# Performance work log

Measured on AMD Instinct MI355X. Metric: run time of the kernel, lower is better.

Reference implementation:

```python
import jax, jax.numpy as jnp
import numpy as np

N = 50000   # nodes
E = 800000  # edges
D = 128     # node_channels


def setup_inputs() -> dict:
    key = jax.random.key(0)
    ks = jax.random.split(key, 16)
    s = 1.0 / np.sqrt(D)
    inp = {
        "x": jax.random.normal(ks[0], (N, D), dtype=jnp.float32),
        "edge_index": jax.random.randint(ks[1], (2, E), 0, N, dtype=jnp.int64),
        "eps": jax.random.normal(ks[2], (N, D), dtype=jnp.float32),
    }
    names = ["1", "2", "mu", "logstd", "5", "6"]
    for i, nm in enumerate(names):
        inp[f"W{nm}"] = jax.random.normal(ks[3 + 2 * i], (D, D), dtype=jnp.float32) * s
        inp[f"b{nm}"] = jnp.zeros((D,), dtype=jnp.float32)
    return inp


def _gcn_norm(edge_index, num_nodes):
    # add self-loops, then symmetric normalization deg^{-1/2} (A+I) deg^{-1/2}
    loop = jnp.arange(num_nodes, dtype=edge_index.dtype)
    src = jnp.concatenate([edge_index[0], loop])
    dst = jnp.concatenate([edge_index[1], loop])
    deg = jax.ops.segment_sum(jnp.ones_like(src, dtype=jnp.float32), dst,
                              num_segments=num_nodes)
    dis = jnp.where(deg > 0, jax.lax.rsqrt(deg), 0.0)
    norm = dis[src] * dis[dst]  # [E + N]
    return src, dst, norm


def _gcn(x, W, b, src, dst, norm, num_nodes):
    h = x @ W                              # [N, D] small GEMM
    msg = h[src] * norm[:, None]           # gather + scale, [E+N, D]
    out = jax.ops.segment_sum(msg, dst, num_segments=num_nodes)  # scatter-add
    return out + b


def reference(x, edge_index, eps, W1, b1, W2, b2, Wmu, bmu, Wlogstd, blogstd,
              W5, b5, W6, b6):
    num_nodes = x.shape[0]
    src, dst, norm = _gcn_norm(edge_index, num_nodes)
    g = lambda h, W, b: _gcn(h, W, b, src, dst, norm, num_nodes)

    nodes = jax.nn.relu(g(x, W1, b1))
    nodes = jax.nn.relu(g(nodes, W2, b2))
    mu = g(nodes, Wmu, bmu)
    logstd = g(nodes, Wlogstd, blogstd)
    # reparametrize (training mode), divider = 10
    nodes = mu + eps * jnp.exp(logstd) / 10.0
    nodes = jax.nn.relu(g(nodes, W5, b5))
    nodes = jax.nn.relu(g(nodes, W6, b6))
    return nodes
```

## Files before the change

### kernel.cpp

```cpp
#include <hip/hip_runtime.h>
#include <hip/hip_bf16.h>
#include <cstdint>
#include <cstddef>

#define D 128
#define NWG 200

typedef _Float16 f16;
typedef f16 f16x2 __attribute__((ext_vector_type(2)));
typedef f16 f16x4 __attribute__((ext_vector_type(4)));
typedef f16 f16x8 __attribute__((ext_vector_type(8)));
typedef float f32x4 __attribute__((ext_vector_type(4)));
typedef unsigned short u16;

static inline size_t align256(size_t x){ return (x + 255) & ~(size_t)255; }

__device__ __forceinline__ int detect_is64(const void* ei){
  const int* e32 = (const int*)ei;
  int probe = e32[2 * (threadIdx.x & 31) + 1];
  return (__ballot(probe != 0) == 0ULL) ? 1 : 0;
}

__device__ __forceinline__ void load_edge(const void* ei, int E, int is64, int e, int& s, int& d){
  if (is64) {
    const long long* p = (const long long*)ei;
    s = (int)p[e]; d = (int)p[(size_t)E + e];
  } else {
    const int* p = (const int*)ei;
    s = p[e]; d = p[(size_t)E + e];
  }
}

__global__ __launch_bounds__(256) void passA_hist(
    const void* __restrict__ ei, int E,
    int* __restrict__ glob_hist, int NB){
  __shared__ int cnt[256];
  int t = threadIdx.x, wg = blockIdx.x;
  int is64 = detect_is64(ei);
  cnt[t] = 0;
  __syncthreads();
  int chunk = (E + NWG - 1) / NWG;
  int lo = wg * chunk, hi = min(lo + chunk, E);
  for (int e = lo + t; e < hi; e += 256){
    int s, d;
    load_edge(ei, E, is64, e, s, d);
    atomicAdd(&cnt[d >> 8], 1);
  }
  __syncthreads();
  for (int b = t; b < NB; b += 256)
    glob_hist[b * NWG + wg] = cnt[b];
}

__global__ void scan_partial(const int* __restrict__ src, int* __restrict__ dst,
                             int* __restrict__ blockSums, int L){
  __shared__ int sd[256];
  int t = threadIdx.x;
  int base = blockIdx.x * 1024 + t * 4;
  int v[4]; int s = 0;
  #pragma unroll
  for (int j = 0; j < 4; ++j){ v[j] = (base + j < L) ? src[base + j] : 0; s += v[j]; }
  sd[t] = s; __syncthreads();
  for (int off = 1; off < 256; off <<= 1){
    int x = (t >= off) ? sd[t - off] : 0;
    __syncthreads();
    sd[t] += x;
    __syncthreads();
  }
  int run = sd[t] - s;
  #pragma unroll
  for (int j = 0; j < 4; ++j){
    if (base + j < L) dst[base + j] = run;
    run += v[j];
  }
  if (t == 255) blockSums[blockIdx.x] = sd[255];
}

__global__ void scan_blocksums(int* __restrict__ blockSums, int nblk){
  __shared__ int sd[256];
  int t = threadIdx.x;
  int v = (t < nblk) ? blockSums[t] : 0;
  sd[t] = v; __syncthreads();
  for (int off = 1; off < 256; off <<= 1){
    int x = (t >= off) ? sd[t - off] : 0;
    __syncthreads();
    sd[t] += x;
    __syncthreads();
  }
  if (t < nblk) blockSums[t] = sd[t] - v;
}

__global__ __launch_bounds__(256) void passB_scatter(
    const void* __restrict__ ei, int E,
    const int* __restrict__ bucketOff, const int* __restrict__ blockSums,
    int NB, unsigned* __restrict__ packed){
  __shared__ int cur[256];
  int t = threadIdx.x, wg = blockIdx.x;
  int is64 = detect_is64(ei);
  for (int b = t; b < NB; b += 256){
    int i = b * NWG + wg;
    cur[b] = bucketOff[i] + blockSums[i >> 10];
  }
  __syncthreads();
  int chunk = (E + NWG - 1) / NWG;
  int lo = wg * chunk, hi = min(lo + chunk, E);
  for (int e = lo + t; e < hi; e += 256){
    int s, d;
    load_edge(ei, E, is64, e, s, d);
    int pos = atomicAdd(&cur[d >> 8], 1);
    packed[pos] = (unsigned)s | ((unsigned)(d & 255) << 16);
  }
}

__global__ __launch_bounds__(256) void passC_csr(
    const unsigned* __restrict__ packed, const int* __restrict__ bucketOff,
    const int* __restrict__ blockSums, int NB, int N, int E,
    int* __restrict__ rowptr, float* __restrict__ dis, u16* __restrict__ csr_src){
  __shared__ int degl[256];
  __shared__ int sd[256];
  __shared__ int cur[256];
  int t = threadIdx.x, b = blockIdx.x;
  int i0 = b * NWG, i1 = (b + 1) * NWG;
  int begin = bucketOff[i0] + blockSums[i0 >> 10];
  int endb  = (b == NB - 1) ? E : (bucketOff[i1] + blockSums[i1 >> 10]);
  degl[t] = 0;
  __syncthreads();
  for (int i = begin + t; i < endb; i += 256)
    atomicAdd(&degl[(packed[i] >> 16) & 255], 1);
  __syncthreads();
  int dv = degl[t];
  sd[t] = dv; __syncthreads();
  for (int off = 1; off < 256; off <<= 1){
    int x = (t >= off) ? sd[t - off] : 0;
    __syncthreads();
    sd[t] += x;
    __syncthreads();
  }
  int localOff = sd[t] - dv;
  int v = b * 256 + t;
  if (v < N){
    rowptr[v] = begin + localOff;
    dis[v] = rsqrtf((float)(dv + 1));
  }
  if (b == NB - 1 && t == 0) rowptr[N] = E;
  cur[t] = begin + localOff;
  __syncthreads();
  for (int i = begin + t; i < endb; i += 256){
    unsigned p = packed[i];
    int pos = atomicAdd(&cur[(p >> 16) & 255], 1);
    csr_src[pos] = (u16)(p & 0xFFFFu);
  }
}

__global__ void cast_scale(const float* __restrict__ in, const float* __restrict__ dis,
                           f16* __restrict__ out, int n4){
  int i = blockIdx.x * blockDim.x + threadIdx.x;
  if (i >= n4) return;
  float dv = dis[i >> 5];
  float4 v = ((const float4*)in)[i];
  f16x4 o; o[0]=(f16)(v.x*dv); o[1]=(f16)(v.y*dv); o[2]=(f16)(v.z*dv); o[3]=(f16)(v.w*dv);
  ((f16x4*)out)[i] = o;
}

__global__ void prep_w(const float* __restrict__ Wa, const float* __restrict__ Wb,
                       const float* __restrict__ Wc, const float* __restrict__ Wd,
                       const float* __restrict__ We, const float* __restrict__ Wf,
                       f16* __restrict__ Wt){
  int i = blockIdx.x * 256 + threadIdx.x;
  int w = i >> 14, rem = i & 16383;
  int n = rem >> 7, k = rem & 127;
  const float* Wp = (w==0)?Wa:(w==1)?Wb:(w==2)?Wc:(w==3)?Wd:(w==4)?We:Wf;
  Wt[i] = (f16)Wp[k*128 + n];
}

__global__ __launch_bounds__(256) void agg16(
    const f16* __restrict__ in, f16* __restrict__ out,
    const int* __restrict__ rowptr, const u16* __restrict__ csr_src,
    const float* __restrict__ dis, int N){
  int v = blockIdx.x * 4 + (threadIdx.x >> 6);
  if (v >= N) return;
  int c2 = (threadIdx.x & 63) * 2;
  float dv = dis[v];
  int beg = rowptr[v], end = rowptr[v + 1];
  f16x2 sv = *(const f16x2*)&in[(size_t)v * D + c2];
  float acc0 = (float)sv[0], acc1 = (float)sv[1];
  int e = beg;
  for (; e + 15 < end; e += 16){
    f16x2 h[16];
    #pragma unroll
    for (int j = 0; j < 16; ++j){
      unsigned u = __builtin_nontemporal_load(&csr_src[e + j]);
      h[j] = *(const f16x2*)&in[(size_t)u * D + c2];
    }
    #pragma unroll
    for (int j = 0; j < 16; ++j){ acc0 += (float)h[j][0]; acc1 += (float)h[j][1]; }
  }
  int rem = end - e;
  if (rem > 0){
    int last = end - 1;
    f16x2 h[16];
    #pragma unroll
    for (int j = 0; j < 16; ++j){
      int idx = e + j;
      idx = idx > last ? last : idx;
      unsigned u = __builtin_nontemporal_load(&csr_src[idx]);
      h[j] = *(const f16x2*)&in[(size_t)u * D + c2];
    }
    #pragma unroll
    for (int j = 0; j < 16; ++j){
      acc0 += (j < rem) ? (float)h[j][0] : 0.f;
      acc1 += (j < rem) ? (float)h[j][1] : 0.f;
    }
  }
  f16x2 o; o[0] = (f16)(acc0 * dv); o[1] = (f16)(acc1 * dv);
  __builtin_nontemporal_store(o, (f16x2*)&out[(size_t)v * D + c2]);
}

template<int EPI>
__global__ __launch_bounds__(512) void gemm_mfma(
    const f16* __restrict__ A, const f16* __restrict__ Wt, const float* __restrict__ bias,
    const f16* __restrict__ Wt2, const float* __restrict__ bias2,
    const float* __restrict__ eps, const float* __restrict__ dis,
    f16* __restrict__ out16, float* __restrict__ outf, int N){

  extern __shared__ __align__(16) f16 Ws[];

  int t = threadIdx.x;
  int wave = t >> 6, lane = t & 63;
  int lrow = lane & 15, hi = lane >> 4;
  int r0 = blockIdx.x * 128 + wave * 16;
  bool active = (r0 < N);

  f16x8 a[4];
  if (active){
    int rr = min(r0 + lrow, N - 1);
    const f16* arow = &A[(size_t)rr * D + hi * 8];
    #pragma unroll
    for (int s = 0; s < 4; ++s) a[s] = *(const f16x8*)&arow[s * 32];
  }

  {
    int r = t & 127, p = t >> 7;
    const float4* src = (const float4*)&Wt[r * 128 + p * 32];
    f16* dstrow = &Ws[r * 128];
    #pragma unroll
    for (int i = 0; i < 4; ++i){
      int q = p * 4 + i;
      *(float4*)&dstrow[(q ^ (r & 7)) * 8] = src[i];
    }
    if (EPI == 1){
      const float4* src2 = (const float4*)&Wt2[r * 128 + p * 32];
      f16* dstrow2 = &Ws[16384 + r * 128];
      #pragma unroll
      for (int i = 0; i < 4; ++i){
        int q = p * 4 + i;
        *(float4*)&dstrow2[(q ^ (r & 7)) * 8] = src2[i];
      }
    }
  }
  __syncthreads();
  if (!active) return;

  f32x4 acc[8] = {};
  f32x4 acc2[8] = {};

  #pragma unroll
  for (int s = 0; s < 4; ++s){
    #pragma unroll
    for (int tt = 0; tt < 8; ++tt){
      int n = tt * 16 + lrow;
      int q = (s * 4 + hi) ^ (lrow & 7);
      f16x8 b = *(const f16x8*)&Ws[n * 128 + q * 8];
      acc[tt] = __builtin_amdgcn_mfma_f32_16x16x32_f16(b, a[s], acc[tt], 0, 0, 0);
      if (EPI == 1){
        f16x8 b2 = *(const f16x8*)&Ws[16384 + n * 128 + q * 8];
        acc2[tt] = __builtin_amdgcn_mfma_f32_16x16x32_f16(b2, a[s], acc2[tt], 0, 0, 0);
      }
    }
  }

  int r = r0 + lrow;
  if (r >= N) return;
  float dv = (EPI == 2) ? 1.f : dis[r];
  int cbase = hi * 4;
  #pragma unroll
  for (int tt = 0; tt < 8; ++tt){
    int n0 = tt * 16 + cbase;
    f32x4 bv = *(const f32x4*)&bias[n0];
    if (EPI == 0){
      f16x4 o;
      #pragma unroll
      for (int ii = 0; ii < 4; ++ii)
        o[ii] = (f16)(fmaxf(acc[tt][ii] + bv[ii], 0.f) * dv);
      *(f16x4*)&out16[(size_t)r * D + n0] = o;
    } else if (EPI == 1){
      f32x4 bv2 = *(const f32x4*)&bias2[n0];
      f32x4 e4  = *(const f32x4*)&eps[(size_t)r * D + n0];
      f16x4 o;
      #pragma unroll
      for (int ii = 0; ii < 4; ++ii){
        float mu = acc[tt][ii] + bv[ii];
        float ls = acc2[tt][ii] + bv2[ii];
        o[ii] = (f16)((mu + e4[ii] * __expf(ls) * 0.1f) * dv);
      }
      *(f16x4*)&out16[(size_t)r * D + n0] = o;
    } else {
      f32x4 o;
      #pragma unroll
      for (int ii = 0; ii < 4; ++ii)
        o[ii] = fmaxf(acc[tt][ii] + bv[ii], 0.f);
      *(f32x4*)&outf[(size_t)r * D + n0] = o;
    }
  }
}

extern "C" void kernel_launch(void* const* d_in, const int* in_sizes, int n_in,
                              void* d_out, int out_size, void* d_ws, size_t ws_size,
                              hipStream_t stream){
  const float* x   = (const float*)d_in[0];
  const void*  ei  = d_in[1];
  const float* eps = (const float*)d_in[2];
  const float* W1  = (const float*)d_in[3];  const float* b1  = (const float*)d_in[4];
  const float* W2  = (const float*)d_in[5];  const float* b2  = (const float*)d_in[6];
  const float* Wmu = (const float*)d_in[7];  const float* bmu = (const float*)d_in[8];
  const float* Wls = (const float*)d_in[9];  const float* bls = (const float*)d_in[10];
  const float* W5  = (const float*)d_in[11]; const float* b5  = (const float*)d_in[12];
  const float* W6  = (const float*)d_in[13]; const float* b6  = (const float*)d_in[14];

  const int N = in_sizes[0] / D;
  const int E = in_sizes[1] / 2;
  const int NB = (N + 255) >> 8;
  const int L  = NB * NWG;
  float* out = (float*)d_out;

  char* ws = (char*)d_ws;
  size_t off = 0;
  auto alloc = [&](size_t bytes){ char* p = ws + off; off += align256(bytes); return p; };
  int*      glob_hist = (int*)     alloc(((size_t)L + 1) * 4);
  int*      bucketOff = (int*)     alloc(((size_t)L + 1) * 4);
  int*      blockSums = (int*)     alloc(1024);
  int*      rowptr    = (int*)     alloc(((size_t)N + 1) * 4);
  float*    dis       = (float*)   alloc((size_t)N * 4);
  unsigned* packed    = (unsigned*)alloc((size_t)E * 4);
  u16*      csr_src   = (u16*)     alloc((size_t)E * 2);
  f16*      Wt        = (f16*)     alloc((size_t)6 * 128 * 128 * 2);
  f16*      bufA      = (f16*)     alloc((size_t)N * D * 2);
  f16*      bufB      = (f16*)     alloc((size_t)N * D * 2);
  (void)ws_size; (void)n_in; (void)out_size;

  passA_hist<<<NWG, 256, 0, stream>>>(ei, E, glob_hist, NB);
  int nblk = (L + 1023) / 1024;
  scan_partial<<<nblk, 256, 0, stream>>>(glob_hist, bucketOff, blockSums, L);
  scan_blocksums<<<1, 256, 0, stream>>>(blockSums, nblk);
  passB_scatter<<<NWG, 256, 0, stream>>>(ei, E, bucketOff, blockSums, NB, packed);
  passC_csr<<<NB, 256, 0, stream>>>(packed, bucketOff, blockSums, NB, N, E, rowptr, dis, csr_src);

  cast_scale<<<(N * D / 4 + 255) / 256, 256, 0, stream>>>(x, dis, bufB, N * D / 4);
  prep_w<<<(6 * 16384) / 256, 256, 0, stream>>>(W1, W2, Wmu, Wls, W5, W6, Wt);

  int aggGrid = (N + 3) / 4;
  int gemmGrid = (N + 127) / 128;
  size_t lds1 = 128 * 128 * sizeof(f16);
  size_t lds2 = 2 * 128 * 128 * sizeof(f16);

  agg16<<<aggGrid, 256, 0, stream>>>(bufB, bufA, rowptr, csr_src, dis, N);
  gemm_mfma<0><<<gemmGrid, 512, lds1, stream>>>(bufA, Wt + 0*16384, b1, nullptr, nullptr, nullptr, dis, bufB, nullptr, N);
  agg16<<<aggGrid, 256, 0, stream>>>(bufB, bufA, rowptr, csr_src, dis, N);
  gemm_mfma<0><<<gemmGrid, 512, lds1, stream>>>(bufA, Wt + 1*16384, b2, nullptr, nullptr, nullptr, dis, bufB, nullptr, N);
  agg16<<<aggGrid, 256, 0, stream>>>(bufB, bufA, rowptr, csr_src, dis, N);
  gemm_mfma<1><<<gemmGrid, 512, lds2, stream>>>(bufA, Wt + 2*16384, bmu, Wt + 3*16384, bls, eps, dis, bufB, nullptr, N);
  agg16<<<aggGrid, 256, 0, stream>>>(bufB, bufA, rowptr, csr_src, dis, N);
  gemm_mfma<0><<<gemmGrid, 512, lds1, stream>>>(bufA, Wt + 4*16384, b5, nullptr, nullptr, nullptr, dis, bufB, nullptr, N);
  agg16<<<aggGrid, 256, 0, stream>>>(bufB, bufA, rowptr, csr_src, dis, N);
  gemm_mfma<2><<<gemmGrid, 512, lds1, stream>>>(bufA, Wt + 5*16384, b6, nullptr, nullptr, nullptr, dis, nullptr, out, N);
}
```

Measured before the change: 385.1 us.

## Fuse neighbor aggregation into the MFMA GEMM kernel per layer

Merges the separate sparse aggregation kernel into the GEMM kernel. Each wave now gathers neighbor rows for its 16 nodes straight into the MFMA A-fragment registers, then runs the dense transform. This removes the intermediate buffer write and read and halves the kernel launches per layer. In exchange, the gather now runs with 16-byte per-lane loads, only 2 edges in flight per iteration and a 512-thread block. That may reduce memory-level parallelism and occupancy compared with the old 16-deep unrolled gather.

```diff
diff --git a/kernel.cpp b/kernel.cpp
--- a/kernel.cpp
+++ b/kernel.cpp
@@ -172,54 +172,13 @@
   Wt[i] = (f16)Wp[k*128 + n];
 }
 
-__global__ __launch_bounds__(256) void agg16(
-    const f16* __restrict__ in, f16* __restrict__ out,
-    const int* __restrict__ rowptr, const u16* __restrict__ csr_src,
-    const float* __restrict__ dis, int N){
-  int v = blockIdx.x * 4 + (threadIdx.x >> 6);
-  if (v >= N) return;
-  int c2 = (threadIdx.x & 63) * 2;
-  float dv = dis[v];
-  int beg = rowptr[v], end = rowptr[v + 1];
-  f16x2 sv = *(const f16x2*)&in[(size_t)v * D + c2];
-  float acc0 = (float)sv[0], acc1 = (float)sv[1];
-  int e = beg;
-  for (; e + 15 < end; e += 16){
-    f16x2 h[16];
-    #pragma unroll
-    for (int j = 0; j < 16; ++j){
-      unsigned u = __builtin_nontemporal_load(&csr_src[e + j]);
-      h[j] = *(const f16x2*)&in[(size_t)u * D + c2];
-    }
-    #pragma unroll
-    for (int j = 0; j < 16; ++j){ acc0 += (float)h[j][0]; acc1 += (float)h[j][1]; }
-  }
-  int rem = end - e;
-  if (rem > 0){
-    int last = end - 1;
-    f16x2 h[16];
-    #pragma unroll
-    for (int j = 0; j < 16; ++j){
-      int idx = e + j;
-      idx = idx > last ? last : idx;
-      unsigned u = __builtin_nontemporal_load(&csr_src[idx]);
-      h[j] = *(const f16x2*)&in[(size_t)u * D + c2];
-    }
-    #pragma unroll
-    for (int j = 0; j < 16; ++j){
-      acc0 += (j < rem) ? (float)h[j][0] : 0.f;
-      acc1 += (j < rem) ? (float)h[j][1] : 0.f;
-    }
-  }
-  f16x2 o; o[0] = (f16)(acc0 * dv); o[1] = (f16)(acc1 * dv);
-  __builtin_nontemporal_store(o, (f16x2*)&out[(size_t)v * D + c2]);
-}
-
 template<int EPI>
-__global__ __launch_bounds__(512) void gemm_mfma(
-    const f16* __restrict__ A, const f16* __restrict__ Wt, const float* __restrict__ bias,
+__global__ __launch_bounds__(512) void agg_gemm(
+    const f16* __restrict__ in,
+    const f16* __restrict__ Wt, const float* __restrict__ bias,
     const f16* __restrict__ Wt2, const float* __restrict__ bias2,
     const float* __restrict__ eps, const float* __restrict__ dis,
+    const int* __restrict__ rowptr, const u16* __restrict__ csr_src,
     f16* __restrict__ out16, float* __restrict__ outf, int N){
 
   extern __shared__ __align__(16) f16 Ws[];
@@ -228,15 +187,6 @@
   int wave = t >> 6, lane = t & 63;
   int lrow = lane & 15, hi = lane >> 4;
   int r0 = blockIdx.x * 128 + wave * 16;
-  bool active = (r0 < N);
-
-  f16x8 a[4];
-  if (active){
-    int rr = min(r0 + lrow, N - 1);
-    const f16* arow = &A[(size_t)rr * D + hi * 8];
-    #pragma unroll
-    for (int s = 0; s < 4; ++s) a[s] = *(const f16x8*)&arow[s * 32];
-  }
 
   {
     int r = t & 127, p = t >> 7;
@@ -257,12 +207,59 @@
       }
     }
   }
-  __syncthreads();
-  if (!active) return;
-
-  f32x4 acc[8] = {};
-  f32x4 acc2[8] = {};
-
+
+  int v = min(r0 + lrow, N - 1);
+  float dv = dis[v];
+  int beg = rowptr[v], end = rowptr[v + 1];
+  const f16* inh = in + hi * 8;
+
+  float acc[4][8];
+  {
+    const f16* vrow = &inh[(size_t)v * D];
+    #pragma unroll
+    for (int s = 0; s < 4; ++s){
+      f16x8 h = *(const f16x8*)&vrow[s * 32];
+      #pragma unroll
+      for (int j = 0; j < 8; ++j) acc[s][j] = (float)h[j];
+    }
+  }
+  int e = beg;
+  for (; e + 1 < end; e += 2){
+    unsigned u0 = __builtin_nontemporal_load(&csr_src[e]);
+    unsigned u1 = __builtin_nontemporal_load(&csr_src[e + 1]);
+    const f16* p0 = &inh[(size_t)u0 * D];
+    const f16* p1 = &inh[(size_t)u1 * D];
+    f16x8 h0[4], h1[4];
+    #pragma unroll
+    for (int s = 0; s < 4; ++s){ h0[s] = *(const f16x8*)&p0[s * 32];
+                                 h1[s] = *(const f16x8*)&p1[s * 32]; }
+    #pragma unroll
+    for (int s = 0; s < 4; ++s)
+      #pragma unroll
+      for (int j = 0; j < 8; ++j)
+        acc[s][j] += (float)h0[s][j] + (float)h1[s][j];
+  }
+  if (e < end){
+    unsigned u = __builtin_nontemporal_load(&csr_src[e]);
+    const f16* p0 = &inh[(size_t)u * D];
+    #pragma unroll
+    for (int s = 0; s < 4; ++s){
+      f16x8 h = *(const f16x8*)&p0[s * 32];
+      #pragma unroll
+      for (int j = 0; j < 8; ++j) acc[s][j] += (float)h[j];
+    }
+  }
+
+  f16x8 a[4];
+  #pragma unroll
+  for (int s = 0; s < 4; ++s)
+    #pragma unroll
+    for (int j = 0; j < 8; ++j) a[s][j] = (f16)(acc[s][j] * dv);
+
+  __syncthreads();
+
+  f32x4 c1[8] = {};
+  f32x4 c2[8] = {};
   #pragma unroll
   for (int s = 0; s < 4; ++s){
     #pragma unroll
@@ -270,17 +267,16 @@
       int n = tt * 16 + lrow;
       int q = (s * 4 + hi) ^ (lrow & 7);
       f16x8 b = *(const f16x8*)&Ws[n * 128 + q * 8];
-      acc[tt] = __builtin_amdgcn_mfma_f32_16x16x32_f16(b, a[s], acc[tt], 0, 0, 0);
+      c1[tt] = __builtin_amdgcn_mfma_f32_16x16x32_f16(b, a[s], c1[tt], 0, 0, 0);
       if (EPI == 1){
         f16x8 b2 = *(const f16x8*)&Ws[16384 + n * 128 + q * 8];
-        acc2[tt] = __builtin_amdgcn_mfma_f32_16x16x32_f16(b2, a[s], acc2[tt], 0, 0, 0);
+        c2[tt] = __builtin_amdgcn_mfma_f32_16x16x32_f16(b2, a[s], c2[tt], 0, 0, 0);
       }
     }
   }
 
   int r = r0 + lrow;
   if (r >= N) return;
-  float dv = (EPI == 2) ? 1.f : dis[r];
   int cbase = hi * 4;
   #pragma unroll
   for (int tt = 0; tt < 8; ++tt){
@@ -290,7 +286,7 @@
       f16x4 o;
       #pragma unroll
       for (int ii = 0; ii < 4; ++ii)
-        o[ii] = (f16)(fmaxf(acc[tt][ii] + bv[ii], 0.f) * dv);
+        o[ii] = (f16)(fmaxf(c1[tt][ii] + bv[ii], 0.f) * dv);
       *(f16x4*)&out16[(size_t)r * D + n0] = o;
     } else if (EPI == 1){
       f32x4 bv2 = *(const f32x4*)&bias2[n0];
@@ -298,8 +294,8 @@
       f16x4 o;
       #pragma unroll
       for (int ii = 0; ii < 4; ++ii){
-        float mu = acc[tt][ii] + bv[ii];
-        float ls = acc2[tt][ii] + bv2[ii];
+        float mu = c1[tt][ii] + bv[ii];
+        float ls = c2[tt][ii] + bv2[ii];
         o[ii] = (f16)((mu + e4[ii] * __expf(ls) * 0.1f) * dv);
       }
       *(f16x4*)&out16[(size_t)r * D + n0] = o;
@@ -307,7 +303,7 @@
       f32x4 o;
       #pragma unroll
       for (int ii = 0; ii < 4; ++ii)
-        o[ii] = fmaxf(acc[tt][ii] + bv[ii], 0.f);
+        o[ii] = fmaxf(c1[tt][ii] + bv[ii], 0.f);
       *(f32x4*)&outf[(size_t)r * D + n0] = o;
     }
   }
@@ -357,19 +353,13 @@
   cast_scale<<<(N * D / 4 + 255) / 256, 256, 0, stream>>>(x, dis, bufB, N * D / 4);
   prep_w<<<(6 * 16384) / 256, 256, 0, stream>>>(W1, W2, Wmu, Wls, W5, W6, Wt);
 
-  int aggGrid = (N + 3) / 4;
-  int gemmGrid = (N + 127) / 128;
+  int grid = (N + 127) / 128;
   size_t lds1 = 128 * 128 * sizeof(f16);
   size_t lds2 = 2 * 128 * 128 * sizeof(f16);
 
-  agg16<<<aggGrid, 256, 0, stream>>>(bufB, bufA, rowptr, csr_src, dis, N);
-  gemm_mfma<0><<<gemmGrid, 512, lds1, stream>>>(bufA, Wt + 0*16384, b1, nullptr, nullptr, nullptr, dis, bufB, nullptr, N);
-  agg16<<<aggGrid, 256, 0, stream>>>(bufB, bufA, rowptr, csr_src, dis, N);
-  gemm_mfma<0><<<gemmGrid, 512, lds1, stream>>>(bufA, Wt + 1*16384, b2, nullptr, nullptr, nullptr, dis, bufB, nullptr, N);
-  agg16<<<aggGrid, 256, 0, stream>>>(bufB, bufA, rowptr, csr_src, dis, N);
-  gemm_mfma<1><<<gemmGrid, 512, lds2, stream>>>(bufA, Wt + 2*16384, bmu, Wt + 3*16384, bls, eps, dis, bufB, nullptr, N);
-  agg16<<<aggGrid, 256, 0, stream>>>(bufB, bufA, rowptr, csr_src, dis, N);
-  gemm_mfma<0><<<gemmGrid, 512, lds1, stream>>>(bufA, Wt + 4*16384, b5, nullptr, nullptr, nullptr, dis, bufB, nullptr, N);
-  agg16<<<aggGrid, 256, 0, stream>>>(bufB, bufA, rowptr, csr_src, dis, N);
-  gemm_mfma<2><<<gemmGrid, 512, lds1, stream>>>(bufA, Wt + 5*16384, b6, nullptr, nullptr, nullptr, dis, nullptr, out, N);
-}
+  agg_gemm<0><<<grid, 512, lds1, stream>>>(bufB, Wt + 0*16384, b1, nullptr, nullptr, nullptr, dis, rowptr, csr_src, bufA, nullptr, N);
+  agg_gemm<0><<<grid, 512, lds1, stream>>>(bufA, Wt + 1*16384, b2, nullptr, nullptr, nullptr, dis, rowptr, csr_src, bufB, nullptr, N);
+  agg_gemm<1><<<grid, 512, lds2, stream>>>(bufB, Wt + 2*16384, bmu, Wt + 3*16384, bls, eps, dis, rowptr, csr_src, bufA, nullptr, N);
+  agg_gemm<0><<<grid, 512, lds1, stream>>>(bufA, Wt + 4*16384, b5, nullptr, nullptr, nullptr, dis, rowptr, csr_src, bufB, nullptr, N);
+  agg_gemm<2><<<grid, 512, lds1, stream>>>(bufB, Wt + 5*16384, b6, nullptr, nullptr, nullptr, dis, rowptr, csr_src, nullptr, out, N);
+}
```

Result: slower. 415.6 us (+7.9%).

## Fuse weight prep and input cast into CSR kernels; split GEMM columns across wave pairs

Applied to the files above, without the earlier changes.

Weight transpose/cast is folded into extra blocks of the histogram kernel, and the x cast-and-scale is folded into the tail of the CSR build kernel using per-node dis values kept in shared memory. This removes two kernel launches. The GEMM now gives each 16-row tile to a pair of waves, each computing half of the output columns, so every block covers 64 rows, the grid doubles and per-wave accumulator registers are halved. The fused cast uses narrower f16x2 accesses and runs on only NB blocks, which may lower bandwidth, and every GEMM block now reloads the full weight matrix into LDS for half as many rows.

```diff
diff --git a/kernel.cpp b/kernel.cpp
--- a/kernel.cpp
+++ b/kernel.cpp
@@ -33,9 +33,21 @@
 
 __global__ __launch_bounds__(256) void passA_hist(
     const void* __restrict__ ei, int E,
-    int* __restrict__ glob_hist, int NB){
+    int* __restrict__ glob_hist, int NB,
+    const float* __restrict__ Wa, const float* __restrict__ Wb,
+    const float* __restrict__ Wc, const float* __restrict__ Wd,
+    const float* __restrict__ We, const float* __restrict__ Wf,
+    f16* __restrict__ Wt){
+  int t = threadIdx.x, wg = blockIdx.x;
+  if (wg >= NWG){
+    int i = (wg - NWG) * 256 + t;
+    int w = i >> 14, rem = i & 16383;
+    int n = rem >> 7, k = rem & 127;
+    const float* Wp = (w==0)?Wa:(w==1)?Wb:(w==2)?Wc:(w==3)?Wd:(w==4)?We:Wf;
+    Wt[i] = (f16)Wp[k*128 + n];
+    return;
+  }
   __shared__ int cnt[256];
-  int t = threadIdx.x, wg = blockIdx.x;
   int is64 = detect_is64(ei);
   cnt[t] = 0;
   __syncthreads();
@@ -114,10 +126,12 @@
 __global__ __launch_bounds__(256) void passC_csr(
     const unsigned* __restrict__ packed, const int* __restrict__ bucketOff,
     const int* __restrict__ blockSums, int NB, int N, int E,
-    int* __restrict__ rowptr, float* __restrict__ dis, u16* __restrict__ csr_src){
+    int* __restrict__ rowptr, float* __restrict__ dis, u16* __restrict__ csr_src,
+    const float* __restrict__ x, f16* __restrict__ bufB){
   __shared__ int degl[256];
   __shared__ int sd[256];
   __shared__ int cur[256];
+  __shared__ float disl[256];
   int t = threadIdx.x, b = blockIdx.x;
   int i0 = b * NWG, i1 = (b + 1) * NWG;
   int begin = bucketOff[i0] + blockSums[i0 >> 10];
@@ -130,16 +144,18 @@
   int dv = degl[t];
   sd[t] = dv; __syncthreads();
   for (int off = 1; off < 256; off <<= 1){
-    int x = (t >= off) ? sd[t - off] : 0;
-    __syncthreads();
-    sd[t] += x;
+    int xm = (t >= off) ? sd[t - off] : 0;
+    __syncthreads();
+    sd[t] += xm;
     __syncthreads();
   }
   int localOff = sd[t] - dv;
   int v = b * 256 + t;
+  float dval = rsqrtf((float)(dv + 1));
+  disl[t] = dval;
   if (v < N){
     rowptr[v] = begin + localOff;
-    dis[v] = rsqrtf((float)(dv + 1));
+    dis[v] = dval;
   }
   if (b == NB - 1 && t == 0) rowptr[N] = E;
   cur[t] = begin + localOff;
@@ -149,27 +165,16 @@
     int pos = atomicAdd(&cur[(p >> 16) & 255], 1);
     csr_src[pos] = (u16)(p & 0xFFFFu);
   }
-}
-
-__global__ void cast_scale(const float* __restrict__ in, const float* __restrict__ dis,
-                           f16* __restrict__ out, int n4){
-  int i = blockIdx.x * blockDim.x + threadIdx.x;
-  if (i >= n4) return;
-  float dv = dis[i >> 5];
-  float4 v = ((const float4*)in)[i];
-  f16x4 o; o[0]=(f16)(v.x*dv); o[1]=(f16)(v.y*dv); o[2]=(f16)(v.z*dv); o[3]=(f16)(v.w*dv);
-  ((f16x4*)out)[i] = o;
-}
-
-__global__ void prep_w(const float* __restrict__ Wa, const float* __restrict__ Wb,
-                       const float* __restrict__ Wc, const float* __restrict__ Wd,
-                       const float* __restrict__ We, const float* __restrict__ Wf,
-                       f16* __restrict__ Wt){
-  int i = blockIdx.x * 256 + threadIdx.x;
-  int w = i >> 14, rem = i & 16383;
-  int n = rem >> 7, k = rem & 127;
-  const float* Wp = (w==0)?Wa:(w==1)?Wb:(w==2)?Wc:(w==3)?Wd:(w==4)?We:Wf;
-  Wt[i] = (f16)Wp[k*128 + n];
+  for (int i = t; i < 256 * 64; i += 256){
+    int vl = i >> 6;
+    int c2 = (i & 63) * 2;
+    int vv = b * 256 + vl;
+    if (vv >= N) break;
+    const float* xr = &x[(size_t)vv * D + c2];
+    float dvv = disl[vl];
+    f16x2 o; o[0] = (f16)(xr[0] * dvv); o[1] = (f16)(xr[1] * dvv);
+    *(f16x2*)&bufB[(size_t)vv * D + c2] = o;
+  }
 }
 
 __global__ __launch_bounds__(256) void agg16(
@@ -227,11 +232,11 @@
   int t = threadIdx.x;
   int wave = t >> 6, lane = t & 63;
   int lrow = lane & 15, hi = lane >> 4;
-  int r0 = blockIdx.x * 128 + wave * 16;
-  bool active = (r0 < N);
+  int pair = wave >> 1, half = wave & 1;
+  int r0 = blockIdx.x * 64 + pair * 16;
 
   f16x8 a[4];
-  if (active){
+  {
     int rr = min(r0 + lrow, N - 1);
     const f16* arow = &A[(size_t)rr * D + hi * 8];
     #pragma unroll
@@ -258,22 +263,21 @@
     }
   }
   __syncthreads();
-  if (!active) return;
-
-  f32x4 acc[8] = {};
-  f32x4 acc2[8] = {};
+
+  f32x4 c1[4] = {};
+  f32x4 c2[4] = {};
 
   #pragma unroll
   for (int s = 0; s < 4; ++s){
     #pragma unroll
-    for (int tt = 0; tt < 8; ++tt){
-      int n = tt * 16 + lrow;
+    for (int tti = 0; tti < 4; ++tti){
+      int n = (half * 4 + tti) * 16 + lrow;
       int q = (s * 4 + hi) ^ (lrow & 7);
       f16x8 b = *(const f16x8*)&Ws[n * 128 + q * 8];
-      acc[tt] = __builtin_amdgcn_mfma_f32_16x16x32_f16(b, a[s], acc[tt], 0, 0, 0);
+      c1[tti] = __builtin_amdgcn_mfma_f32_16x16x32_f16(b, a[s], c1[tti], 0, 0, 0);
       if (EPI == 1){
         f16x8 b2 = *(const f16x8*)&Ws[16384 + n * 128 + q * 8];
-        acc2[tt] = __builtin_amdgcn_mfma_f32_16x16x32_f16(b2, a[s], acc2[tt], 0, 0, 0);
+        c2[tti] = __builtin_amdgcn_mfma_f32_16x16x32_f16(b2, a[s], c2[tti], 0, 0, 0);
       }
     }
   }
@@ -283,14 +287,14 @@
   float dv = (EPI == 2) ? 1.f : dis[r];
   int cbase = hi * 4;
   #pragma unroll
-  for (int tt = 0; tt < 8; ++tt){
-    int n0 = tt * 16 + cbase;
+  for (int tti = 0; tti < 4; ++tti){
+    int n0 = (half * 4 + tti) * 16 + cbase;
     f32x4 bv = *(const f32x4*)&bias[n0];
     if (EPI == 0){
       f16x4 o;
       #pragma unroll
       for (int ii = 0; ii < 4; ++ii)
-        o[ii] = (f16)(fmaxf(acc[tt][ii] + bv[ii], 0.f) * dv);
+        o[ii] = (f16)(fmaxf(c1[tti][ii] + bv[ii], 0.f) * dv);
       *(f16x4*)&out16[(size_t)r * D + n0] = o;
     } else if (EPI == 1){
       f32x4 bv2 = *(const f32x4*)&bias2[n0];
@@ -298,8 +302,8 @@
       f16x4 o;
       #pragma unroll
       for (int ii = 0; ii < 4; ++ii){
-        float mu = acc[tt][ii] + bv[ii];
-        float ls = acc2[tt][ii] + bv2[ii];
+        float mu = c1[tti][ii] + bv[ii];
+        float ls = c2[tti][ii] + bv2[ii];
         o[ii] = (f16)((mu + e4[ii] * __expf(ls) * 0.1f) * dv);
       }
       *(f16x4*)&out16[(size_t)r * D + n0] = o;
@@ -307,7 +311,7 @@
       f32x4 o;
       #pragma unroll
       for (int ii = 0; ii < 4; ++ii)
-        o[ii] = fmaxf(acc[tt][ii] + bv[ii], 0.f);
+        o[ii] = fmaxf(c1[tti][ii] + bv[ii], 0.f);
       *(f32x4*)&outf[(size_t)r * D + n0] = o;
     }
   }
@@ -347,18 +351,17 @@
   f16*      bufB      = (f16*)     alloc((size_t)N * D * 2);
   (void)ws_size; (void)n_in; (void)out_size;
 
-  passA_hist<<<NWG, 256, 0, stream>>>(ei, E, glob_hist, NB);
+  passA_hist<<<NWG + 384, 256, 0, stream>>>(ei, E, glob_hist, NB,
+                                            W1, W2, Wmu, Wls, W5, W6, Wt);
   int nblk = (L + 1023) / 1024;
   scan_partial<<<nblk, 256, 0, stream>>>(glob_hist, bucketOff, blockSums, L);
   scan_blocksums<<<1, 256, 0, stream>>>(blockSums, nblk);
   passB_scatter<<<NWG, 256, 0, stream>>>(ei, E, bucketOff, blockSums, NB, packed);
-  passC_csr<<<NB, 256, 0, stream>>>(packed, bucketOff, blockSums, NB, N, E, rowptr, dis, csr_src);
-
-  cast_scale<<<(N * D / 4 + 255) / 256, 256, 0, stream>>>(x, dis, bufB, N * D / 4);
-  prep_w<<<(6 * 16384) / 256, 256, 0, stream>>>(W1, W2, Wmu, Wls, W5, W6, Wt);
+  passC_csr<<<NB, 256, 0, stream>>>(packed, bucketOff, blockSums, NB, N, E,
+                                    rowptr, dis, csr_src, x, bufB);
 
   int aggGrid = (N + 3) / 4;
-  int gemmGrid = (N + 127) / 128;
+  int gemmGrid = (N + 63) / 64;
   size_t lds1 = 128 * 128 * sizeof(f16);
   size_t lds2 = 2 * 128 * 128 * sizeof(f16);
 
```

Result: slower. 422.8 us (+9.8%).
